# Optimization experiments

Measured on AMD Instinct MI355X. Metric: run time of the kernel, lower is better.

Reference implementation:

```python
import jax, jax.numpy as jnp
import numpy as np

HIDDEN = 1024
NUM_HEADS = 16
HEAD_DIM = HIDDEN // NUM_HEADS


def setup_inputs() -> dict:
    key = jax.random.key(0)
    k1, k2, k3 = jax.random.split(key, 3)
    x = jax.random.normal(k1, (2, 2048, HIDDEN), dtype=jnp.float32)
    # Linear weights, torch layout [out_features, in_features]
    w_qkv = jax.random.normal(k2, (3 * HIDDEN, HIDDEN), dtype=jnp.float32) * 0.02
    w_out = jax.random.normal(k3, (HIDDEN, HIDDEN), dtype=jnp.float32) * 0.02
    return {"x": x, "w_qkv": w_qkv, "w_out": w_out}


def reference(x, w_qkv, w_out):
    B, S, H = x.shape
    scale = 1.0 / HEAD_DIM ** 0.5
    qkv = jnp.einsum('bsh,oh->bso', x, w_qkv)              # [B,S,3H]
    qkv = qkv.reshape(B, S, 3, NUM_HEADS, HEAD_DIM)
    qkv = jnp.transpose(qkv, (2, 0, 3, 1, 4))               # [3,B,nh,S,hd]
    q, k, v = qkv[0], qkv[1], qkv[2]
    scores = jnp.einsum('bnsd,bntd->bnst', q, k) * scale    # [B,nh,S,S]
    attn = jax.nn.softmax(scores, axis=-1)
    out = jnp.einsum('bnst,bntd->bnsd', attn, v)            # [B,nh,S,hd]
    out = jnp.transpose(out, (0, 2, 1, 3)).reshape(B, S, H)
    return jnp.einsum('bsh,oh->bso', out, w_out)
```

## Files before the change

### kernel.cpp

```cpp
#include <hip/hip_runtime.h>
#include <stdint.h>

typedef unsigned short u16;
typedef __bf16 bf16x8 __attribute__((ext_vector_type(8)));
typedef float f32x4 __attribute__((ext_vector_type(4)));
typedef float f32x16 __attribute__((ext_vector_type(16)));
typedef unsigned u32x4 __attribute__((ext_vector_type(4)));

#define DEVI __device__ __forceinline__

typedef __attribute__((address_space(1))) void gvoid;
typedef __attribute__((address_space(3))) void lvoid;

DEVI u16 f2b(float f) {
  unsigned x = __builtin_bit_cast(unsigned, f);
  return (u16)((x + 0x7fffu + ((x >> 16) & 1u)) >> 16);
}

DEVI float exp2g(float x) { return __builtin_amdgcn_exp2f(x); }

DEVI void gload_lds16(const void* g, void* l) {
  __builtin_amdgcn_global_load_lds((gvoid*)g, (lvoid*)l, 16, 0, 0);
}

#define QSCALE 0.18033688011112042f

__global__ void cast_x(const float* __restrict__ in, u16* __restrict__ out, int n4) {
  int i = blockIdx.x * 256 + threadIdx.x;
  int stride = gridDim.x * 256;
  for (; i < n4; i += stride) {
    float4 v = ((const float4*)in)[i];
    ushort4 o;
    o.x = f2b(v.x); o.y = f2b(v.y); o.z = f2b(v.z); o.w = f2b(v.w);
    ((ushort4*)out)[i] = o;
  }
}

__global__ void cast_w(const float* __restrict__ wqkv, const float* __restrict__ wout,
                       u16* __restrict__ outb) {
  int i = blockIdx.x * 256 + threadIdx.x;
  int stride = gridDim.x * 256;
  for (; i < 1048576; i += stride) {
    const float* src = (i < 786432) ? wqkv + 4 * (long)i : wout + 4 * (long)(i - 786432);
    float4 v = *(const float4*)src;
    if (i < 262144) { v.x *= QSCALE; v.y *= QSCALE; v.z *= QSCALE; v.w *= QSCALE; }
    ushort4 o;
    o.x = f2b(v.x); o.y = f2b(v.y); o.z = f2b(v.z); o.w = f2b(v.w);
    ((ushort4*)outb)[i] = o;
  }
}

template<int OUT, int TM>
__global__ __launch_bounds__(256)
void gemm_bt(const u16* __restrict__ A, const u16* __restrict__ B, void* __restrict__ Cv,
             void* __restrict__ Cv2, int M, int N, int K) {
  constexpr int MI = TM / 32;
  __shared__ u16 lA[TM * 64];
  __shared__ u16 lB[128 * 64];
  const int tid = threadIdx.x;
  const int lane = tid & 63;
  const int lr = lane & 15;
  const int lg = lane >> 4;
  const int wid = tid >> 6;
  const long bm = (long)blockIdx.y * TM;
  const long bn = (long)blockIdx.x * 128;
  const int wr = (wid >> 1) * (TM / 2);
  const int wc = (wid & 1) * 64;

  f32x4 acc[MI][4];
#pragma unroll
  for (int i = 0; i < MI; ++i)
#pragma unroll
    for (int j = 0; j < 4; ++j)
      acc[i][j] = (f32x4){0.f, 0.f, 0.f, 0.f};

  for (int k0 = 0; k0 < K; k0 += 64) {
#pragma unroll
    for (int q = 0; q < MI; ++q) {
      int bi = tid + q * 256;
      int row = bi >> 3;
      int col = ((bi & 7) ^ (row & 7)) * 8;
      gload_lds16(A + (bm + row) * (long)K + k0 + col, (char*)lA + bi * 16);
    }
#pragma unroll
    for (int q = 0; q < 4; ++q) {
      int bi = tid + q * 256;
      int row = bi >> 3;
      int col = ((bi & 7) ^ (row & 7)) * 8;
      gload_lds16(B + (bn + row) * (long)K + k0 + col, (char*)lB + bi * 16);
    }
    __syncthreads();
#pragma unroll
    for (int kk = 0; kk < 2; ++kk) {
      bf16x8 af[MI], bfr[4];
      int kb = kk * 4 + lg;
#pragma unroll
      for (int mi = 0; mi < MI; ++mi) {
        int row = wr + mi * 16 + lr;
        af[mi] = *(const bf16x8*)((const char*)lA + row * 128 + ((kb ^ (row & 7)) << 4));
      }
#pragma unroll
      for (int ni = 0; ni < 4; ++ni) {
        int row = wc + ni * 16 + lr;
        bfr[ni] = *(const bf16x8*)((const char*)lB + row * 128 + ((kb ^ (row & 7)) << 4));
      }
#pragma unroll
      for (int mi = 0; mi < MI; ++mi)
#pragma unroll
        for (int ni = 0; ni < 4; ++ni)
          acc[mi][ni] = __builtin_amdgcn_mfma_f32_16x16x32_bf16(af[mi], bfr[ni], acc[mi][ni], 0, 0, 0);
    }
    __syncthreads();
  }

  if (OUT == 2 && bn >= 2048) {
#pragma unroll
    for (int mi = 0; mi < MI; ++mi)
#pragma unroll
      for (int ni = 0; ni < 4; ++ni) {
        long tok = bm + wr + mi * 16 + lg * 4;
        long f = bn + wc + ni * 16 + lr - 2048;
        ushort4 st;
        st.x = f2b(acc[mi][ni][0]);
        st.y = f2b(acc[mi][ni][1]);
        st.z = f2b(acc[mi][ni][2]);
        st.w = f2b(acc[mi][ni][3]);
        u16* dst = (u16*)Cv2 + (((tok >> 11) << 4) + (f >> 6)) * 131072 + (f & 63) * 2048 + (tok & 2047);
        *(ushort4*)dst = st;
      }
  } else {
    const long strideN = (OUT == 2) ? 2048 : N;
#pragma unroll
    for (int mi = 0; mi < MI; ++mi)
#pragma unroll
      for (int ni = 0; ni < 4; ++ni)
#pragma unroll
        for (int r = 0; r < 4; ++r) {
          long row = bm + wr + mi * 16 + lg * 4 + r;
          long col = bn + wc + ni * 16 + lr;
          float v = acc[mi][ni][r];
          if (OUT == 1) ((float*)Cv)[row * strideN + col] = v;
          else          ((u16*)Cv)[row * strideN + col] = f2b(v);
        }
  }
}

__global__ __launch_bounds__(512, 4)
void attn_fwd(const u16* __restrict__ qk, const u16* __restrict__ vT,
              u16* __restrict__ outb) {
  __shared__ char SM[65536];

  const int tid = threadIdx.x;
  const int lane = tid & 63;
  const int wid = tid >> 6;
  const int ql = lane & 31;
  const int h  = lane >> 5;
  const int th = wid >> 2;
  const int qb = wid & 3;

  const int flat = blockIdx.x + (blockIdx.y << 4) + (blockIdx.z << 8);
  const int swz  = ((flat & 7) << 6) + (flat >> 3);
  const int qt = swz & 15;
  const int hd = (swz >> 4) & 15;
  const int b  = swz >> 8;

  const long rowbase = (long)b * 2048;
  const int qcol = hd * 64;
  const int kcol = 1024 + hd * 64;
  const int TK = 128 * 2048;
  const long vhb = ((long)b * 16 + hd) * 131072;

  const int q0w = qt * 128 + qb * 32;
  bf16x8 qf[4];
  {
    const u16* qp = qk + (rowbase + q0w + ql) * 2048 + qcol + h * 8;
#pragma unroll
    for (int dblk = 0; dblk < 4; ++dblk)
      qf[dblk] = *(const bf16x8*)(qp + dblk * 16);
  }

  float l_r = 0.f;
  f32x16 o[2];
#pragma unroll
  for (int d = 0; d < 2; ++d)
#pragma unroll
    for (int r = 0; r < 16; ++r) o[d][r] = 0.f;

  const int rk = tid >> 3;
  const int ck = ((tid & 7) ^ (rk & 7)) * 8;
  const int dstb = tid * 16;
  const u16* kp = qk + (rowbase + rk) * 2048 + kcol + ck;
  const u16* vp = vT + vhb + rk * 2048 + ck;

  gload_lds16(kp,             SM + dstb);
  gload_lds16(kp + 64 * 2048, SM + 8192 + dstb);
  gload_lds16(vp,             SM + 32768 + dstb);
  gload_lds16(vp + 64,        SM + 40960 + dstb);
  kp += TK; vp += 128;
  asm volatile("s_waitcnt vmcnt(0)" ::: "memory");
  __builtin_amdgcn_s_barrier();
  __builtin_amdgcn_sched_barrier(0);

  for (int tt = 0; tt < 8; ++tt) {
#pragma unroll
    for (int P = 0; P < 2; ++P) {
      char* KsCur = SM + P * 16384;
      char* VsCur = SM + 32768 + P * 16384;
      char* KsNxt = SM + (P ^ 1) * 16384;
      char* VsNxt = SM + 32768 + (P ^ 1) * 16384;

      gload_lds16(kp,             KsNxt + dstb);
      gload_lds16(kp + 64 * 2048, KsNxt + 8192 + dstb);
      gload_lds16(vp,             VsNxt + dstb);
      gload_lds16(vp + 64,        VsNxt + 8192 + dstb);
      kp += TK; vp += 128;

#pragma unroll
      for (int j = 0; j < 2; ++j) {
        f32x16 s;
#pragma unroll
        for (int r = 0; r < 16; ++r) s[r] = 0.f;
        const char* Kb = KsCur + j * 8192 + (th * 32 + ql) * 128;
        __builtin_amdgcn_s_setprio(1);
#pragma unroll
        for (int kd = 0; kd < 4; ++kd) {
          bf16x8 kf = *(const bf16x8*)(Kb + (((kd * 2 + h) ^ (ql & 7)) << 4));
          s = __builtin_amdgcn_mfma_f32_32x32x16_bf16(kf, qf[kd], s, 0, 0, 0);
        }
        __builtin_amdgcn_s_setprio(0);

#pragma unroll
        for (int r = 0; r < 16; ++r) s[r] = exp2g(s[r]);
        l_r += (((s[0] + s[1]) + (s[2] + s[3])) + ((s[4] + s[5]) + (s[6] + s[7])))
             + (((s[8] + s[9]) + (s[10] + s[11])) + ((s[12] + s[13]) + (s[14] + s[15])));

        unsigned w[8];
#pragma unroll
        for (int m = 0; m < 8; ++m)
          asm("v_cvt_pk_bf16_f32 %0, %1, %2" : "=v"(w[m]) : "v"(s[2 * m]), "v"(s[2 * m + 1]));

        bf16x8 pb[2];
#pragma unroll
        for (int ks = 0; ks < 2; ++ks) {
          unsigned a0 = w[4 * ks],     a2 = w[4 * ks + 2];
          unsigned a1 = w[4 * ks + 1], a3 = w[4 * ks + 3];
          asm("s_nop 1\n\tv_permlane32_swap_b32 %0, %1" : "+v"(a0), "+v"(a2));
          asm("s_nop 1\n\tv_permlane32_swap_b32 %0, %1" : "+v"(a1), "+v"(a3));
          u32x4 t; t[0] = a0; t[1] = a1; t[2] = a2; t[3] = a3;
          pb[ks] = __builtin_bit_cast(bf16x8, t);
        }

        __builtin_amdgcn_s_setprio(1);
#pragma unroll
        for (int dblk = 0; dblk < 2; ++dblk) {
          const char* Vb = VsCur + j * 8192 + (dblk * 32 + ql) * 128;
#pragma unroll
          for (int ks = 0; ks < 2; ++ks) {
            bf16x8 vf = *(const bf16x8*)(Vb + (((th * 4 + ks * 2 + h) ^ (ql & 7)) << 4));
            o[dblk] = __builtin_amdgcn_mfma_f32_32x32x16_bf16(vf, pb[ks], o[dblk], 0, 0, 0);
          }
        }
        __builtin_amdgcn_s_setprio(0);
      }

      asm volatile("s_waitcnt vmcnt(0)" ::: "memory");
      __builtin_amdgcn_s_barrier();
      __builtin_amdgcn_sched_barrier(0);
    }
  }
  __syncthreads();

  float px = l_r, py = l_r;
  asm("s_nop 1\n\tv_permlane32_swap_b32 %0, %1" : "+v"(px), "+v"(py));
  float lw = l_r + (h ? px : py);

  if (th == 1) {
    char* reg = SM + qb * 8320;
#pragma unroll
    for (int dblk = 0; dblk < 2; ++dblk)
#pragma unroll
      for (int r = 0; r < 16; ++r) {
        int dl = dblk * 32 + (r & 3) + 8 * (r >> 2) + 4 * h;
        *(float*)(reg + dl * 128 + ql * 4) = o[dblk][r];
      }
    if (h == 0) *(float*)(reg + 8192 + ql * 4) = lw;
  }
  __syncthreads();
  if (th == 0) {
    const char* reg = SM + qb * 8320;
#pragma unroll
    for (int dblk = 0; dblk < 2; ++dblk)
#pragma unroll
      for (int r = 0; r < 16; ++r) {
        int dl = dblk * 32 + (r & 3) + 8 * (r >> 2) + 4 * h;
        o[dblk][r] += *(const float*)(reg + dl * 128 + ql * 4);
      }
    float inv = 1.0f / (lw + *(const float*)(reg + 8192 + ql * 4));
    long row = rowbase + q0w + ql;
#pragma unroll
    for (int dblk = 0; dblk < 2; ++dblk)
#pragma unroll
      for (int m = 0; m < 4; ++m) {
        ushort4 st;
        st.x = f2b(o[dblk][4 * m + 0] * inv);
        st.y = f2b(o[dblk][4 * m + 1] * inv);
        st.z = f2b(o[dblk][4 * m + 2] * inv);
        st.w = f2b(o[dblk][4 * m + 3] * inv);
        *(ushort4*)(outb + row * 1024 + qcol + dblk * 32 + 8 * m + 4 * h) = st;
      }
  }
}

extern "C" void kernel_launch(void* const* d_in, const int* in_sizes, int n_in,
                              void* d_out, int out_size, void* d_ws, size_t ws_size,
                              hipStream_t stream) {
  const float* x     = (const float*)d_in[0];
  const float* w_qkv = (const float*)d_in[1];
  const float* w_out = (const float*)d_in[2];
  float* out = (float*)d_out;

  char* ws = (char*)d_ws;
  u16* xb    = (u16*)(ws);
  u16* wqkvb = (u16*)(ws + 8388608);
  u16* woutb = (u16*)(ws + 14680064);
  u16* qk    = (u16*)(ws + 16777216);
  u16* vT    = (u16*)(ws + 33554432);
  u16* attn  = (u16*)(ws + 41943040);

  cast_x<<<1024, 256, 0, stream>>>(x, xb, 4096 * 1024 / 4);
  cast_w<<<1024, 256, 0, stream>>>(w_qkv, w_out, wqkvb);

  gemm_bt<2, 128><<<dim3(24, 32), 256, 0, stream>>>(xb, wqkvb, qk, vT, 4096, 3072, 1024);

  attn_fwd<<<dim3(16, 16, 2), 512, 0, stream>>>(qk, vT, attn);

  gemm_bt<1, 64><<<dim3(8, 64), 256, 0, stream>>>(attn, woutb, out, nullptr, 4096, 1024, 1024);
}
```

Before: 105.3 us.

## Halve attention block size and merge input cast kernels into one launch

The attention kernel now uses 256-thread blocks covering 64 query rows with 64-key K/V tiles and 32KB LDS, launched over twice as many blocks. This raises the block count and lowers LDS use per block, aiming for better occupancy and load balance. The cost is that each K/V tile is reused by fewer query rows, so more global traffic per output. Separately, the x and weight cast kernels are fused into a single launch to save one kernel launch.

```diff
diff --git a/kernel.cpp b/kernel.cpp
--- a/kernel.cpp
+++ b/kernel.cpp
@@ -25,27 +25,25 @@
 
 #define QSCALE 0.18033688011112042f
 
-__global__ void cast_x(const float* __restrict__ in, u16* __restrict__ out, int n4) {
+__global__ void cast_all(const float* __restrict__ x, const float* __restrict__ wqkv,
+                         const float* __restrict__ wout, u16* __restrict__ outb) {
   int i = blockIdx.x * 256 + threadIdx.x;
   int stride = gridDim.x * 256;
-  for (; i < n4; i += stride) {
-    float4 v = ((const float4*)in)[i];
+  for (; i < 2097152; i += stride) {
+    const float* src;
+    float sc = 1.0f;
+    if (i < 1048576) {
+      src = x + 4 * (long)i;
+    } else if (i < 1835008) {
+      int j = i - 1048576;
+      src = wqkv + 4 * (long)j;
+      if (j < 262144) sc = QSCALE;
+    } else {
+      src = wout + 4 * (long)(i - 1835008);
+    }
+    float4 v = *(const float4*)src;
     ushort4 o;
-    o.x = f2b(v.x); o.y = f2b(v.y); o.z = f2b(v.z); o.w = f2b(v.w);
-    ((ushort4*)out)[i] = o;
-  }
-}
-
-__global__ void cast_w(const float* __restrict__ wqkv, const float* __restrict__ wout,
-                       u16* __restrict__ outb) {
-  int i = blockIdx.x * 256 + threadIdx.x;
-  int stride = gridDim.x * 256;
-  for (; i < 1048576; i += stride) {
-    const float* src = (i < 786432) ? wqkv + 4 * (long)i : wout + 4 * (long)(i - 786432);
-    float4 v = *(const float4*)src;
-    if (i < 262144) { v.x *= QSCALE; v.y *= QSCALE; v.z *= QSCALE; v.w *= QSCALE; }
-    ushort4 o;
-    o.x = f2b(v.x); o.y = f2b(v.y); o.z = f2b(v.z); o.w = f2b(v.w);
+    o.x = f2b(v.x * sc); o.y = f2b(v.y * sc); o.z = f2b(v.z * sc); o.w = f2b(v.w * sc);
     ((ushort4*)outb)[i] = o;
   }
 }
@@ -145,32 +143,32 @@
   }
 }
 
-__global__ __launch_bounds__(512, 4)
+__global__ __launch_bounds__(256, 4)
 void attn_fwd(const u16* __restrict__ qk, const u16* __restrict__ vT,
               u16* __restrict__ outb) {
-  __shared__ char SM[65536];
+  __shared__ char SM[32768];
 
   const int tid = threadIdx.x;
   const int lane = tid & 63;
   const int wid = tid >> 6;
   const int ql = lane & 31;
   const int h  = lane >> 5;
-  const int th = wid >> 2;
-  const int qb = wid & 3;
-
-  const int flat = blockIdx.x + (blockIdx.y << 4) + (blockIdx.z << 8);
-  const int swz  = ((flat & 7) << 6) + (flat >> 3);
-  const int qt = swz & 15;
-  const int hd = (swz >> 4) & 15;
-  const int b  = swz >> 8;
+  const int th = wid >> 1;
+  const int qb = wid & 1;
+
+  const int flat = blockIdx.x + (blockIdx.y << 5) + (blockIdx.z << 9);
+  const int swz  = ((flat & 7) << 7) + (flat >> 3);
+  const int qt = swz & 31;
+  const int hd = (swz >> 5) & 15;
+  const int b  = swz >> 9;
 
   const long rowbase = (long)b * 2048;
   const int qcol = hd * 64;
   const int kcol = 1024 + hd * 64;
-  const int TK = 128 * 2048;
+  const int TSK = 64 * 2048;
   const long vhb = ((long)b * 16 + hd) * 131072;
 
-  const int q0w = qt * 128 + qb * 32;
+  const int q0w = qt * 64 + qb * 32;
   bf16x8 qf[4];
   {
     const u16* qp = qk + (rowbase + q0w + ql) * 2048 + qcol + h * 8;
@@ -186,82 +184,78 @@
 #pragma unroll
     for (int r = 0; r < 16; ++r) o[d][r] = 0.f;
 
-  const int rk = tid >> 3;
-  const int ck = ((tid & 7) ^ (rk & 7)) * 8;
-  const int dstb = tid * 16;
-  const u16* kp = qk + (rowbase + rk) * 2048 + kcol + ck;
-  const u16* vp = vT + vhb + rk * 2048 + ck;
-
-  gload_lds16(kp,             SM + dstb);
-  gload_lds16(kp + 64 * 2048, SM + 8192 + dstb);
-  gload_lds16(vp,             SM + 32768 + dstb);
-  gload_lds16(vp + 64,        SM + 40960 + dstb);
-  kp += TK; vp += 128;
+  const int c0 = tid, c1 = tid + 256;
+  const int rk0 = c0 >> 3, ck0 = ((c0 & 7) ^ (rk0 & 7)) * 8;
+  const int rk1 = c1 >> 3, ck1 = ((c1 & 7) ^ (rk1 & 7)) * 8;
+  const int d0 = c0 * 16, d1 = c1 * 16;
+  const u16* kp0 = qk + (rowbase + rk0) * 2048 + kcol + ck0;
+  const u16* kp1 = qk + (rowbase + rk1) * 2048 + kcol + ck1;
+  const u16* vp0 = vT + vhb + rk0 * 2048 + ck0;
+  const u16* vp1 = vT + vhb + rk1 * 2048 + ck1;
+
+  gload_lds16(kp0, SM + d0);          gload_lds16(kp1, SM + d1);
+  gload_lds16(vp0, SM + 16384 + d0);  gload_lds16(vp1, SM + 16384 + d1);
+  kp0 += TSK; kp1 += TSK; vp0 += 64; vp1 += 64;
   asm volatile("s_waitcnt vmcnt(0)" ::: "memory");
   __builtin_amdgcn_s_barrier();
   __builtin_amdgcn_sched_barrier(0);
 
-  for (int tt = 0; tt < 8; ++tt) {
+  for (int tt = 0; tt < 16; ++tt) {
 #pragma unroll
     for (int P = 0; P < 2; ++P) {
-      char* KsCur = SM + P * 16384;
-      char* VsCur = SM + 32768 + P * 16384;
-      char* KsNxt = SM + (P ^ 1) * 16384;
-      char* VsNxt = SM + 32768 + (P ^ 1) * 16384;
-
-      gload_lds16(kp,             KsNxt + dstb);
-      gload_lds16(kp + 64 * 2048, KsNxt + 8192 + dstb);
-      gload_lds16(vp,             VsNxt + dstb);
-      gload_lds16(vp + 64,        VsNxt + 8192 + dstb);
-      kp += TK; vp += 128;
-
-#pragma unroll
-      for (int j = 0; j < 2; ++j) {
-        f32x16 s;
-#pragma unroll
-        for (int r = 0; r < 16; ++r) s[r] = 0.f;
-        const char* Kb = KsCur + j * 8192 + (th * 32 + ql) * 128;
-        __builtin_amdgcn_s_setprio(1);
-#pragma unroll
-        for (int kd = 0; kd < 4; ++kd) {
-          bf16x8 kf = *(const bf16x8*)(Kb + (((kd * 2 + h) ^ (ql & 7)) << 4));
-          s = __builtin_amdgcn_mfma_f32_32x32x16_bf16(kf, qf[kd], s, 0, 0, 0);
+      char* KsCur = SM + P * 8192;
+      char* VsCur = SM + 16384 + P * 8192;
+      char* KsNxt = SM + (P ^ 1) * 8192;
+      char* VsNxt = SM + 16384 + (P ^ 1) * 8192;
+
+      gload_lds16(kp0, KsNxt + d0);  gload_lds16(kp1, KsNxt + d1);
+      gload_lds16(vp0, VsNxt + d0);  gload_lds16(vp1, VsNxt + d1);
+      kp0 += TSK; kp1 += TSK; vp0 += 64; vp1 += 64;
+
+      f32x16 s;
+#pragma unroll
+      for (int r = 0; r < 16; ++r) s[r] = 0.f;
+      const char* Kb = KsCur + (th * 32 + ql) * 128;
+      __builtin_amdgcn_s_setprio(1);
+#pragma unroll
+      for (int kd = 0; kd < 4; ++kd) {
+        bf16x8 kf = *(const bf16x8*)(Kb + (((kd * 2 + h) ^ (ql & 7)) << 4));
+        s = __builtin_amdgcn_mfma_f32_32x32x16_bf16(kf, qf[kd], s, 0, 0, 0);
+      }
+      __builtin_amdgcn_s_setprio(0);
+
+#pragma unroll
+      for (int r = 0; r < 16; ++r) s[r] = exp2g(s[r]);
+      l_r += (((s[0] + s[1]) + (s[2] + s[3])) + ((s[4] + s[5]) + (s[6] + s[7])))
+           + (((s[8] + s[9]) + (s[10] + s[11])) + ((s[12] + s[13]) + (s[14] + s[15])));
+
+      unsigned w[8];
+#pragma unroll
+      for (int m = 0; m < 8; ++m)
+        asm("v_cvt_pk_bf16_f32 %0, %1, %2" : "=v"(w[m]) : "v"(s[2 * m]), "v"(s[2 * m + 1]));
+
+      bf16x8 pb[2];
+#pragma unroll
+      for (int ks = 0; ks < 2; ++ks) {
+        unsigned a0 = w[4 * ks],     a2 = w[4 * ks + 2];
+        unsigned a1 = w[4 * ks + 1], a3 = w[4 * ks + 3];
+        asm("s_nop 1\n\tv_permlane32_swap_b32 %0, %1" : "+v"(a0), "+v"(a2));
+        asm("s_nop 1\n\tv_permlane32_swap_b32 %0, %1" : "+v"(a1), "+v"(a3));
+        u32x4 t; t[0] = a0; t[1] = a1; t[2] = a2; t[3] = a3;
+        pb[ks] = __builtin_bit_cast(bf16x8, t);
+      }
+
+      __builtin_amdgcn_s_setprio(1);
+#pragma unroll
+      for (int dblk = 0; dblk < 2; ++dblk) {
+        const char* Vb = VsCur + (dblk * 32 + ql) * 128;
+#pragma unroll
+        for (int ks = 0; ks < 2; ++ks) {
+          bf16x8 vf = *(const bf16x8*)(Vb + (((th * 4 + ks * 2 + h) ^ (ql & 7)) << 4));
+          o[dblk] = __builtin_amdgcn_mfma_f32_32x32x16_bf16(vf, pb[ks], o[dblk], 0, 0, 0);
         }
-        __builtin_amdgcn_s_setprio(0);
-
-#pragma unroll
-        for (int r = 0; r < 16; ++r) s[r] = exp2g(s[r]);
-        l_r += (((s[0] + s[1]) + (s[2] + s[3])) + ((s[4] + s[5]) + (s[6] + s[7])))
-             + (((s[8] + s[9]) + (s[10] + s[11])) + ((s[12] + s[13]) + (s[14] + s[15])));
-
-        unsigned w[8];
-#pragma unroll
-        for (int m = 0; m < 8; ++m)
-          asm("v_cvt_pk_bf16_f32 %0, %1, %2" : "=v"(w[m]) : "v"(s[2 * m]), "v"(s[2 * m + 1]));
-
-        bf16x8 pb[2];
-#pragma unroll
-        for (int ks = 0; ks < 2; ++ks) {
-          unsigned a0 = w[4 * ks],     a2 = w[4 * ks + 2];
-          unsigned a1 = w[4 * ks + 1], a3 = w[4 * ks + 3];
-          asm("s_nop 1\n\tv_permlane32_swap_b32 %0, %1" : "+v"(a0), "+v"(a2));
-          asm("s_nop 1\n\tv_permlane32_swap_b32 %0, %1" : "+v"(a1), "+v"(a3));
-          u32x4 t; t[0] = a0; t[1] = a1; t[2] = a2; t[3] = a3;
-          pb[ks] = __builtin_bit_cast(bf16x8, t);
-        }
-
-        __builtin_amdgcn_s_setprio(1);
-#pragma unroll
-        for (int dblk = 0; dblk < 2; ++dblk) {
-          const char* Vb = VsCur + j * 8192 + (dblk * 32 + ql) * 128;
-#pragma unroll
-          for (int ks = 0; ks < 2; ++ks) {
-            bf16x8 vf = *(const bf16x8*)(Vb + (((th * 4 + ks * 2 + h) ^ (ql & 7)) << 4));
-            o[dblk] = __builtin_amdgcn_mfma_f32_32x32x16_bf16(vf, pb[ks], o[dblk], 0, 0, 0);
-          }
-        }
-        __builtin_amdgcn_s_setprio(0);
-      }
+      }
+      __builtin_amdgcn_s_setprio(0);
 
       asm volatile("s_waitcnt vmcnt(0)" ::: "memory");
       __builtin_amdgcn_s_barrier();
@@ -327,12 +321,11 @@
   u16* vT    = (u16*)(ws + 33554432);
   u16* attn  = (u16*)(ws + 41943040);
 
-  cast_x<<<1024, 256, 0, stream>>>(x, xb, 4096 * 1024 / 4);
-  cast_w<<<1024, 256, 0, stream>>>(w_qkv, w_out, wqkvb);
+  cast_all<<<2048, 256, 0, stream>>>(x, w_qkv, w_out, xb);
 
   gemm_bt<2, 128><<<dim3(24, 32), 256, 0, stream>>>(xb, wqkvb, qk, vT, 4096, 3072, 1024);
 
-  attn_fwd<<<dim3(16, 16, 2), 512, 0, stream>>>(qk, vT, attn);
+  attn_fwd<<<dim3(32, 16, 2), 256, 0, stream>>>(qk, vT, attn);
 
   gemm_bt<1, 64><<<dim3(8, 64), 256, 0, stream>>>(attn, woutb, out, nullptr, 4096, 1024, 1024);
 }
```

After: 106.6 us. No clear change (+1.2%).
